# Performance work log

Hardware: AMD Instinct MI355X
Metric: run time of the kernel (lower is better)

Reference implementation:

```python
import jax, jax.numpy as jnp
import numpy as np

B, S, D, H = 2, 2048, 512, 8
DK = D // H
MASK_VALUE = -1e9


def setup_inputs() -> dict:
    key = jax.random.key(0)
    ks = jax.random.split(key, 12)
    scale = 1.0 / np.sqrt(D)
    inp = {
        "query": jax.random.normal(ks[0], (B, S, D), jnp.float32),
        "key": jax.random.normal(ks[1], (B, S, D), jnp.float32),
        "value": jax.random.normal(ks[2], (B, S, D), jnp.float32),
        # causal mask, broadcastable over batch and heads
        "mask": jnp.tril(jnp.ones((S, S), jnp.int32))[None, None, :, :],
        "Wq": jax.random.normal(ks[3], (D, D), jnp.float32) * scale,
        "bq": jax.random.normal(ks[4], (D,), jnp.float32) * scale,
        "Wk": jax.random.normal(ks[5], (D, D), jnp.float32) * scale,
        "bk": jax.random.normal(ks[6], (D,), jnp.float32) * scale,
        "Wv": jax.random.normal(ks[7], (D, D), jnp.float32) * scale,
        "bv": jax.random.normal(ks[8], (D,), jnp.float32) * scale,
        "Wo": jax.random.normal(ks[9], (D, D), jnp.float32) * scale,
        "bo": jax.random.normal(ks[10], (D,), jnp.float32) * scale,
    }
    return inp


def reference(query, key, value, mask, Wq, bq, Wk, bk, Wv, bv, Wo, bo):
    # linear projections (torch Linear: x @ W.T + b)
    q = query @ Wq.T + bq
    k = key @ Wk.T + bk
    v = value @ Wv.T + bv
    # split heads: [B,S,D] -> [B,H,S,DK]
    q = q.reshape(B, S, H, DK).transpose(0, 2, 1, 3)
    k = k.reshape(B, S, H, DK).transpose(0, 2, 1, 3)
    v = v.reshape(B, S, H, DK).transpose(0, 2, 1, 3)
    # scaled dot-product attention with explicit [B,H,S,S] score matrix
    scores = jnp.einsum("bhqd,bhkd->bhqk", q, k) / jnp.sqrt(jnp.float32(DK))
    scores = jnp.where(mask == 0, jnp.float32(MASK_VALUE), scores)
    attn = jax.nn.softmax(scores, axis=-1)
    x = jnp.einsum("bhqk,bhkd->bhqd", attn, v)
    # merge heads: [B,H,S,DK] -> [B,S,D]
    x = x.transpose(0, 2, 1, 3).reshape(B, S, D)
    return x @ Wo.T + bo
```

## Files before the change

### kernel.cpp

```cpp
#include <hip/hip_runtime.h>
#include <hip/hip_bf16.h>

#define B_   2
#define S_   2048
#define D_   512
#define H_   8
#define DK_  64
#define M_   (B_*S_)

typedef float  floatx4 __attribute__((ext_vector_type(4)));
typedef __bf16 bf16x8  __attribute__((ext_vector_type(8)));

#define MFMA16x16x32(a,b,c) __builtin_amdgcn_mfma_f32_16x16x32_bf16((a),(b),(c),0,0,0)

static __device__ __forceinline__ void load_lds16(const void* g, void* l) {
  __builtin_amdgcn_global_load_lds(
      (const __attribute__((address_space(1))) void*)g,
      (__attribute__((address_space(3))) void*)l,
      16, 0, 0);
}

__global__ __launch_bounds__(256) void cvt_inputs(
    const float* __restrict__ w0, const float* __restrict__ w1,
    const float* __restrict__ w2, const float* __restrict__ w3,
    const float* __restrict__ x0, const float* __restrict__ x1,
    const float* __restrict__ x2,
    __bf16* __restrict__ out)
{
  const int idx = (blockIdx.x * 256 + threadIdx.x) * 4;
  const float* src;
  int off;
  if (idx < 1048576) {
    src = (idx < 524288) ? ((idx < 262144) ? w0 : w1)
                         : ((idx < 786432) ? w2 : w3);
    off = idx & 0x3FFFF;
  } else {
    const int i2 = idx - 1048576;
    const int xs = i2 >> 21;
    src = (xs == 0) ? x0 : (xs == 1) ? x1 : x2;
    off = i2 & 0x1FFFFF;
  }
  float4 v = *(const float4*)(src + off);
  __bf16* o = out + idx;
  o[0]=(__bf16)v.x; o[1]=(__bf16)v.y; o[2]=(__bf16)v.z; o[3]=(__bf16)v.w;
}


__global__ __launch_bounds__(256) void proj_qkv(
    const __bf16* __restrict__ Xb, const __bf16* __restrict__ Wball,
    const float* __restrict__ bq, const float* __restrict__ bk, const float* __restrict__ bv,
    __bf16* __restrict__ Qb, __bf16* __restrict__ Kb, __bf16* __restrict__ Vtb)
{
  __shared__ __align__(16) __bf16 smem[12288];

  const int z = blockIdx.z;
  const __bf16* X    = Xb + (size_t)z * (M_*D_);
  const __bf16* W    = Wball + (size_t)z * (D_*D_);
  const float*  bias = (z==0) ? bq : (z==1) ? bk : bv;

  const int m0 = blockIdx.x * 64;
  const int n0 = blockIdx.y * 128;
  const int tid  = threadIdx.x;
  const int w    = tid >> 6;
  const int lane = tid & 63;
  const int lcol = lane & 15;
  const int quad = lane >> 4;
  const int wm = w & 1, wn = w >> 1;

  floatx4 zero = {0.f,0.f,0.f,0.f};
  floatx4 acc[2][4];
#pragma unroll
  for (int i = 0; i < 2; ++i)
#pragma unroll
    for (int nt = 0; nt < 4; ++nt) acc[i][nt] = zero;

  auto stage = [&](int bsel, int k0) {
    {
      const int u = w*64 + lane;
      load_lds16(X + (size_t)(m0 + (u >> 2))*D_ + k0 + (u & 3)*8,
                 (char*)(smem + bsel*2048) + w*1024);
    }
#pragma unroll
    for (int j = 0; j < 2; ++j) {
      const int u = (j*4 + w)*64 + lane;
      load_lds16(W + (size_t)(n0 + (u >> 2))*D_ + k0 + (u & 3)*8,
                 (char*)(smem + 4096 + bsel*4096) + (j*4 + w)*1024);
    }
  };

  stage(0, 0);
  for (int it = 0; it < 16; ++it) {
    __syncthreads();
    if (it + 1 < 16) stage((it+1)&1, (it+1)*32);
    const __bf16* ab = smem + (it&1)*2048;
    const __bf16* bb = smem + 4096 + (it&1)*4096;
    bf16x8 af[2], bf[4];
#pragma unroll
    for (int i = 0; i < 2; ++i)
      af[i] = *(const bf16x8*)(ab + (wm*32 + i*16 + lcol)*32 + quad*8);
#pragma unroll
    for (int nt = 0; nt < 4; ++nt)
      bf[nt] = *(const bf16x8*)(bb + (wn*64 + nt*16 + lcol)*32 + quad*8);
#pragma unroll
    for (int i = 0; i < 2; ++i)
#pragma unroll
      for (int nt = 0; nt < 4; ++nt)
        acc[i][nt] = MFMA16x16x32(af[i], bf[nt], acc[i][nt]);
  }

  __syncthreads();
#pragma unroll
  for (int nt = 0; nt < 4; ++nt) {
    const int n = n0 + wn*64 + nt*16 + lcol;
    const float bias_n = bias[n];
    const int h_l = (n >> 6) & 1;
    const int dk  = n & 63;
#pragma unroll
    for (int i = 0; i < 2; ++i)
#pragma unroll
      for (int r = 0; r < 4; ++r) {
        const int m = m0 + wm*32 + i*16 + quad*4 + r;
        const float val = acc[i][nt][r] + bias_n;
        const int klo = m & 63;
        int off;
        if (z == 0) {
          off = klo*64 + dk;
        } else if (z == 1) {
          off = (((klo>>4)*2 + (dk>>5))*64 + ((dk>>3)&3)*16 + (klo&15))*8 + (dk&7);
        } else {
          off = (((dk>>4)*2 + (klo>>5))*64 + ((klo>>3)&3)*16 + (dk&15))*8 + (klo&7);
        }
        smem[h_l*4096 + off] = (__bf16)val;
      }
  }
  __syncthreads();

  __bf16* dst = (z==0) ? Qb : (z==1) ? Kb : Vtb;
  const int bb2 = m0 >> 11;
  const int hh0 = n0 >> 6;
  const int cc0 = (m0 & 2047) >> 6;
#pragma unroll
  for (int it2 = 0; it2 < 4; ++it2) {
    const int u = it2*256 + tid;
    const int p = u >> 9, o = u & 511;
    const size_t base = ((size_t)(bb2*H_ + hh0 + p))*(S_*DK_) + (size_t)cc0*4096;
    *(bf16x8*)(dst + base + o*8) = *(const bf16x8*)(smem + p*4096 + o*8);
  }
}

__global__ __launch_bounds__(256) void attn_fwd(
    const __bf16* __restrict__ Qb, const __bf16* __restrict__ Kb,
    const __bf16* __restrict__ Vtb, __bf16* __restrict__ attnb)
{
  __shared__ __align__(16) __bf16 kbuf[2][4096];
  __shared__ __align__(16) __bf16 vbuf[2][4096];
  __shared__ __align__(16) __bf16 pbuf[4][16*72];

  const int tid  = threadIdx.x;
  const int w    = tid >> 6;
  const int lane = tid & 63;
  const int lcol = lane & 15;
  const int quad = lane >> 4;
  const int hh = blockIdx.y;
  const int bb = blockIdx.z;

  const int t   = (bb == 0) ? (31 - (int)blockIdx.x) : (int)blockIdx.x;
  const int q0  = t * 64;
  const int qr0 = q0 + w*16;

  const __bf16* Qp = Qb  + (size_t)(bb*H_ + hh) * S_ * DK_;
  const __bf16* Kp = Kb  + (size_t)(bb*H_ + hh) * S_ * DK_;
  const __bf16* Vp = Vtb + (size_t)(bb*H_ + hh) * DK_ * S_;

  const bf16x8 aq0 = *(const bf16x8*)(Qp + (size_t)(qr0 + lcol)*DK_ + quad*8);
  const bf16x8 aq1 = *(const bf16x8*)(Qp + (size_t)(qr0 + lcol)*DK_ + 32 + quad*8);

  floatx4 zero = {0.f,0.f,0.f,0.f};
  floatx4 acc[4] = {zero, zero, zero, zero};
  float lsum[4] = {0.f, 0.f, 0.f, 0.f};

  auto stage_chunk = [&](int bsel, int c) {
    const char* ksrc = (const char*)(Kp + (size_t)c * 4096);
    const char* vsrc = (const char*)(Vp + (size_t)c * 4096);
#pragma unroll
    for (int j = 0; j < 2; ++j) {
      const int off = w*2048 + j*1024;
      load_lds16(ksrc + off + lane*16, (char*)kbuf[bsel] + off);
      load_lds16(vsrc + off + lane*16, (char*)vbuf[bsel] + off);
    }
  };

  const int nch = t + 1;
  stage_chunk(0, 0);
  for (int c = 0; c < nch; ++c) {
    __syncthreads();
    if (c + 1 < nch) stage_chunk((c+1)&1, c+1);
    const int bsel = c & 1;
    const int k0 = c * 64;
    const __bf16* kb = kbuf[bsel];
    const __bf16* vb = vbuf[bsel];

    floatx4 s[4];
#pragma unroll
    for (int nt = 0; nt < 4; ++nt) {
      bf16x8 kf0 = *(const bf16x8*)(kb + (nt*2+0)*512 + lane*8);
      bf16x8 kf1 = *(const bf16x8*)(kb + (nt*2+1)*512 + lane*8);
      s[nt] = MFMA16x16x32(aq1, kf1, MFMA16x16x32(aq0, kf0, zero));
    }

    const bool edge = (k0 + 63 > qr0);
#pragma unroll
    for (int nt = 0; nt < 4; ++nt) {
#pragma unroll
      for (int r = 0; r < 4; ++r) {
        float p = exp2f(s[nt][r] * 0.18033688011112042f);
        if (edge) {
          const int qrow = qr0 + quad*4 + r;
          if (k0 + nt*16 + lcol > qrow) p = 0.f;
        }
        lsum[r] += p;
        pbuf[w][(quad*4 + r)*72 + nt*16 + lcol] = (__bf16)p;
      }
    }
    asm volatile("s_waitcnt lgkmcnt(0)" ::: "memory");

    const bf16x8 pa0 = *(const bf16x8*)(&pbuf[w][lcol*72 + quad*8]);
    const bf16x8 pa1 = *(const bf16x8*)(&pbuf[w][lcol*72 + 32 + quad*8]);
#pragma unroll
    for (int nt = 0; nt < 4; ++nt) {
      bf16x8 vf0 = *(const bf16x8*)(vb + (nt*2+0)*512 + lane*8);
      bf16x8 vf1 = *(const bf16x8*)(vb + (nt*2+1)*512 + lane*8);
      acc[nt] = MFMA16x16x32(pa0, vf0, acc[nt]);
      acc[nt] = MFMA16x16x32(pa1, vf1, acc[nt]);
    }
  }

  float rinv[4];
#pragma unroll
  for (int r = 0; r < 4; ++r) {
    float tv = lsum[r];
    tv += __shfl_xor(tv, 1, 16);
    tv += __shfl_xor(tv, 2, 16);
    tv += __shfl_xor(tv, 4, 16);
    tv += __shfl_xor(tv, 8, 16);
    rinv[r] = 1.0f / tv;
  }

#pragma unroll
  for (int nt = 0; nt < 4; ++nt)
#pragma unroll
    for (int r = 0; r < 4; ++r) {
      const int q = qr0 + quad*4 + r;
      attnb[((size_t)(bb*S_ + q)) * D_ + hh*DK_ + nt*16 + lcol] =
          (__bf16)(acc[nt][r] * rinv[r]);
    }
}

__global__ __launch_bounds__(256) void proj_out(
    const __bf16* __restrict__ attnb, const __bf16* __restrict__ Wob,
    const float* __restrict__ bo, float* __restrict__ out)
{
  __shared__ __align__(16) __bf16 smem[12288];

  const int m0 = blockIdx.x * 64;
  const int n0 = blockIdx.y * 128;
  const int tid  = threadIdx.x;
  const int w    = tid >> 6;
  const int lane = tid & 63;
  const int lcol = lane & 15;
  const int quad = lane >> 4;
  const int wm = w & 1, wn = w >> 1;

  floatx4 zero = {0.f,0.f,0.f,0.f};
  floatx4 acc[2][4];
#pragma unroll
  for (int i = 0; i < 2; ++i)
#pragma unroll
    for (int nt = 0; nt < 4; ++nt) acc[i][nt] = zero;

  auto stage = [&](int bsel, int k0) {
    {
      const int u = w*64 + lane;
      load_lds16(attnb + (size_t)(m0 + (u >> 2))*D_ + k0 + (u & 3)*8,
                 (char*)(smem + bsel*2048) + w*1024);
    }
#pragma unroll
    for (int j = 0; j < 2; ++j) {
      const int u = (j*4 + w)*64 + lane;
      load_lds16(Wob + (size_t)(n0 + (u >> 2))*D_ + k0 + (u & 3)*8,
                 (char*)(smem + 4096 + bsel*4096) + (j*4 + w)*1024);
    }
  };

  stage(0, 0);
  for (int it = 0; it < 16; ++it) {
    __syncthreads();
    if (it + 1 < 16) stage((it+1)&1, (it+1)*32);
    const __bf16* ab = smem + (it&1)*2048;
    const __bf16* bb = smem + 4096 + (it&1)*4096;
    bf16x8 af[2], bf[4];
#pragma unroll
    for (int i = 0; i < 2; ++i)
      af[i] = *(const bf16x8*)(ab + (wm*32 + i*16 + lcol)*32 + quad*8);
#pragma unroll
    for (int nt = 0; nt < 4; ++nt)
      bf[nt] = *(const bf16x8*)(bb + (wn*64 + nt*16 + lcol)*32 + quad*8);
#pragma unroll
    for (int i = 0; i < 2; ++i)
#pragma unroll
      for (int nt = 0; nt < 4; ++nt)
        acc[i][nt] = MFMA16x16x32(af[i], bf[nt], acc[i][nt]);
  }

#pragma unroll
  for (int nt = 0; nt < 4; ++nt) {
    const int n = n0 + wn*64 + nt*16 + lcol;
    const float bias_n = bo[n];
#pragma unroll
    for (int i = 0; i < 2; ++i)
#pragma unroll
      for (int r = 0; r < 4; ++r) {
        const int m = m0 + wm*32 + i*16 + quad*4 + r;
        out[(size_t)m * D_ + n] = acc[i][nt][r] + bias_n;
      }
  }
}

extern "C" void kernel_launch(void* const* d_in, const int* in_sizes, int n_in,
                              void* d_out, int out_size, void* d_ws, size_t ws_size,
                              hipStream_t stream) {
  const float* q_in = (const float*)d_in[0];
  const float* k_in = (const float*)d_in[1];
  const float* v_in = (const float*)d_in[2];
  const float* Wq = (const float*)d_in[4];
  const float* bq = (const float*)d_in[5];
  const float* Wk = (const float*)d_in[6];
  const float* bk = (const float*)d_in[7];
  const float* Wv = (const float*)d_in[8];
  const float* bv = (const float*)d_in[9];
  const float* Wo = (const float*)d_in[10];
  const float* bo = (const float*)d_in[11];
  float* out = (float*)d_out;

  __bf16* ws    = (__bf16*)d_ws;
  __bf16* Qb    = ws;
  __bf16* Kb    = ws + 1*2097152;
  __bf16* Vtb   = ws + 2*2097152;
  __bf16* attnb = ws + 3*2097152;
  __bf16* Wb    = ws + 4*2097152;
  __bf16* Xb    = Wb + 4*262144;

  cvt_inputs<<<dim3(7168), dim3(256), 0, stream>>>(
      Wq, Wk, Wv, Wo, q_in, k_in, v_in, Wb);

  proj_qkv<<<dim3(M_/64, D_/128, 3), dim3(256), 0, stream>>>(
      Xb, Wb, bq, bk, bv, Qb, Kb, Vtb);

  attn_fwd<<<dim3(32, H_, B_), dim3(256), 0, stream>>>(Qb, Kb, Vtb, attnb);

  proj_out<<<dim3(M_/64, D_/128), dim3(256), 0, stream>>>(
      attnb, Wb + 3*262144, bo, out);
}
```

Baseline: 171.3 us.

## Split causal attention KV range across blocks with separate reduce kernel

Long query tiles now have their causal KV range split into segments of up to 8 chunks, each handled by its own block. Partial unnormalized outputs and row sums go to a workspace reused from the converted-input buffer, and a new reduce kernel sums the segments and normalizes. This balances the triangular workload and raises the block count from 512 to 1280. The cost is an extra kernel launch plus writing and reading the bf16 partials. The softmax already skips the max subtraction, so partials can be summed directly.

```diff
diff --git a/kernel.cpp b/kernel.cpp
--- a/kernel.cpp
+++ b/kernel.cpp
@@ -150,7 +150,8 @@
 
 __global__ __launch_bounds__(256) void attn_fwd(
     const __bf16* __restrict__ Qb, const __bf16* __restrict__ Kb,
-    const __bf16* __restrict__ Vtb, __bf16* __restrict__ attnb)
+    const __bf16* __restrict__ Vtb, __bf16* __restrict__ attnb,
+    __bf16* __restrict__ Pb, float* __restrict__ Lb)
 {
   __shared__ __align__(16) __bf16 kbuf[2][4096];
   __shared__ __align__(16) __bf16 vbuf[2][4096];
@@ -164,7 +165,16 @@
   const int hh = blockIdx.y;
   const int bb = blockIdx.z;
 
-  const int t   = (bb == 0) ? (31 - (int)blockIdx.x) : (int)blockIdx.x;
+  const int wid = blockIdx.x;
+  int t, s;
+  if (wid < 8)       { t = wid;                  s = 0; }
+  else if (wid < 24) { int u = wid - 8;  t = 8  + (u>>1); s = u & 1; }
+  else if (wid < 48) { int u = wid - 24; int q3 = u/3; t = 16 + q3; s = u - 3*q3; }
+  else               { int u = wid - 48; t = 24 + (u>>2); s = u & 3; }
+  const bool single = (wid < 8);
+
+  const int cbeg = s*8;
+  const int cend = (cbeg + 8 < t + 1) ? (cbeg + 8) : (t + 1);
   const int q0  = t * 64;
   const int qr0 = q0 + w*16;
 
@@ -190,22 +200,21 @@
     }
   };
 
-  const int nch = t + 1;
-  stage_chunk(0, 0);
-  for (int c = 0; c < nch; ++c) {
+  stage_chunk(0, cbeg);
+  for (int c = cbeg; c < cend; ++c) {
     __syncthreads();
-    if (c + 1 < nch) stage_chunk((c+1)&1, c+1);
-    const int bsel = c & 1;
+    if (c + 1 < cend) stage_chunk((c - cbeg + 1)&1, c+1);
+    const int bsel = (c - cbeg) & 1;
     const int k0 = c * 64;
     const __bf16* kb = kbuf[bsel];
     const __bf16* vb = vbuf[bsel];
 
-    floatx4 s[4];
+    floatx4 sc[4];
 #pragma unroll
     for (int nt = 0; nt < 4; ++nt) {
       bf16x8 kf0 = *(const bf16x8*)(kb + (nt*2+0)*512 + lane*8);
       bf16x8 kf1 = *(const bf16x8*)(kb + (nt*2+1)*512 + lane*8);
-      s[nt] = MFMA16x16x32(aq1, kf1, MFMA16x16x32(aq0, kf0, zero));
+      sc[nt] = MFMA16x16x32(aq1, kf1, MFMA16x16x32(aq0, kf0, zero));
     }
 
     const bool edge = (k0 + 63 > qr0);
@@ -213,7 +222,7 @@
     for (int nt = 0; nt < 4; ++nt) {
 #pragma unroll
       for (int r = 0; r < 4; ++r) {
-        float p = exp2f(s[nt][r] * 0.18033688011112042f);
+        float p = exp2f(sc[nt][r] * 0.18033688011112042f);
         if (edge) {
           const int qrow = qr0 + quad*4 + r;
           if (k0 + nt*16 + lcol > qrow) p = 0.f;
@@ -235,25 +244,84 @@
     }
   }
 
-  float rinv[4];
+  float tv[4];
 #pragma unroll
   for (int r = 0; r < 4; ++r) {
-    float tv = lsum[r];
-    tv += __shfl_xor(tv, 1, 16);
-    tv += __shfl_xor(tv, 2, 16);
-    tv += __shfl_xor(tv, 4, 16);
-    tv += __shfl_xor(tv, 8, 16);
-    rinv[r] = 1.0f / tv;
-  }
-
-#pragma unroll
-  for (int nt = 0; nt < 4; ++nt)
-#pragma unroll
-    for (int r = 0; r < 4; ++r) {
-      const int q = qr0 + quad*4 + r;
-      attnb[((size_t)(bb*S_ + q)) * D_ + hh*DK_ + nt*16 + lcol] =
-          (__bf16)(acc[nt][r] * rinv[r]);
-    }
+    float v = lsum[r];
+    v += __shfl_xor(v, 1, 16);
+    v += __shfl_xor(v, 2, 16);
+    v += __shfl_xor(v, 4, 16);
+    v += __shfl_xor(v, 8, 16);
+    tv[r] = v;
+  }
+
+  if (single) {
+#pragma unroll
+    for (int nt = 0; nt < 4; ++nt)
+#pragma unroll
+      for (int r = 0; r < 4; ++r) {
+        const int q = qr0 + quad*4 + r;
+        attnb[((size_t)(bb*S_ + q)) * D_ + hh*DK_ + nt*16 + lcol] =
+            (__bf16)(acc[nt][r] / tv[r]);
+      }
+  } else {
+    const int g = t >> 3;
+    const int basec = (g == 2) ? 16 : ((g == 3) ? 40 : 0);
+    const int pidx = (bb*H_ + hh)*72 + basec + (t - 8*g)*(g + 1) + s;
+
+#pragma unroll
+    for (int nt = 0; nt < 4; ++nt)
+#pragma unroll
+      for (int r = 0; r < 4; ++r)
+        pbuf[w][(quad*4 + r)*72 + nt*16 + lcol] = (__bf16)acc[nt][r];
+    asm volatile("s_waitcnt lgkmcnt(0)" ::: "memory");
+
+    __bf16* pdst = Pb + (size_t)pidx*4096 + w*16*64;
+#pragma unroll
+    for (int i = 0; i < 2; ++i) {
+      const int unit = i*64 + lane;
+      const int row = unit >> 3, grp = unit & 7;
+      *(bf16x8*)(pdst + row*64 + grp*8) =
+          *(const bf16x8*)(&pbuf[w][row*72 + grp*8]);
+    }
+    if (lcol == 0) {
+#pragma unroll
+      for (int r = 0; r < 4; ++r)
+        Lb[(size_t)pidx*64 + w*16 + quad*4 + r] = tv[r];
+    }
+  }
+}
+
+__global__ __launch_bounds__(256) void attn_reduce(
+    const __bf16* __restrict__ Pb, const float* __restrict__ Lb,
+    __bf16* __restrict__ attnb)
+{
+  const int t  = 8 + blockIdx.x;
+  const int bh = blockIdx.y;
+  const int bb = bh >> 3, hh = bh & 7;
+  const int g = t >> 3;
+  const int basec = (g == 2) ? 16 : ((g == 3) ? 40 : 0);
+  const int nseg = g + 1;
+  const int pidx0 = bh*72 + basec + (t - 8*g)*nseg;
+
+#pragma unroll
+  for (int i = 0; i < 2; ++i) {
+    const int unit = i*256 + threadIdx.x;
+    const int row = unit >> 3, grp = unit & 7;
+    float sum[8] = {0,0,0,0,0,0,0,0};
+    float l = 0.f;
+    for (int s2 = 0; s2 < nseg; ++s2) {
+      bf16x8 v = *(const bf16x8*)(Pb + (size_t)(pidx0 + s2)*4096 + row*64 + grp*8);
+#pragma unroll
+      for (int j = 0; j < 8; ++j) sum[j] += (float)v[j];
+      l += Lb[(size_t)(pidx0 + s2)*64 + row];
+    }
+    const float rinv = 1.0f / l;
+    bf16x8 o;
+#pragma unroll
+    for (int j = 0; j < 8; ++j) o[j] = (__bf16)(sum[j] * rinv);
+    *(bf16x8*)(attnb + ((size_t)(bb*S_ + t*64 + row))*D_ + hh*DK_ + grp*8) = o;
+  }
 }
 
 __global__ __launch_bounds__(256) void proj_out(
@@ -350,13 +418,19 @@
   __bf16* Wb    = ws + 4*2097152;
   __bf16* Xb    = Wb + 4*262144;
 
+  __bf16* Pb = Xb;
+  float*  Lb = (float*)(Xb + 1152*4096);
+
   cvt_inputs<<<dim3(7168), dim3(256), 0, stream>>>(
       Wq, Wk, Wv, Wo, q_in, k_in, v_in, Wb);
 
   proj_qkv<<<dim3(M_/64, D_/128, 3), dim3(256), 0, stream>>>(
       Xb, Wb, bq, bk, bv, Qb, Kb, Vtb);
 
-  attn_fwd<<<dim3(32, H_, B_), dim3(256), 0, stream>>>(Qb, Kb, Vtb, attnb);
+  attn_fwd<<<dim3(80, H_, B_), dim3(256), 0, stream>>>(
+      Qb, Kb, Vtb, attnb, Pb, Lb);
+
+  attn_reduce<<<dim3(24, 16), dim3(256), 0, stream>>>(Pb, Lb, attnb);
 
   proj_out<<<dim3(M_/64, D_/128), dim3(256), 0, stream>>>(
       attnb, Wb + 3*262144, bo, out);
```

After: 164.1 us. -4.2%, faster.
